# Optimization experiments

Hardware: AMD Instinct MI355X
Metric: run time of the kernel (lower is better)

## Reference

```python
import math
import jax, jax.numpy as jnp
import numpy as np

C1, D, NUM_HEADS, K_CH = 150, 32, 4, 10
GLOBAL_TOPK_RATIO = 0.08


def _pos2d(h, w, dim):
    d2 = dim // 2
    div = jnp.exp(jnp.arange(0, d2, 2, dtype=jnp.float32) * (-(math.log(10000.0) / d2)))
    def axis_pe(n):
        ang = jnp.arange(n, dtype=jnp.float32)[:, None] * div[None, :]
        pe = jnp.zeros((n, d2), dtype=jnp.float32)
        pe = pe.at[:, 0::2].set(jnp.sin(ang))
        pe = pe.at[:, 1::2].set(jnp.cos(ang))
        return pe
    pe_y = axis_pe(h)  # [h, d2]
    pe_x = axis_pe(w)  # [w, d2]
    return jnp.concatenate([
        jnp.broadcast_to(pe_y[:, None, :], (h, w, d2)),
        jnp.broadcast_to(pe_x[None, :, :], (h, w, d2)),
    ], axis=-1)  # [h, w, dim]


def setup_inputs() -> dict:
    key = jax.random.key(0)
    ks = jax.random.split(key, 7)
    B = 1024
    return {
        "x": jax.random.uniform(ks[0], (B, 1, 28, 28), dtype=jnp.float32),
        "conv1_w": jax.random.normal(ks[1], (C1, 1, 9, 9), dtype=jnp.float32) * 0.05,
        "channel_embed": jax.random.normal(ks[2], (C1, D), dtype=jnp.float32) * 0.02,
        "in_proj_w": jax.random.normal(ks[3], (3 * D, D), dtype=jnp.float32) * (1.0 / math.sqrt(D)),
        "in_proj_b": jnp.zeros((3 * D,), dtype=jnp.float32),
        "out_proj_w": jax.random.normal(ks[4], (D, D), dtype=jnp.float32) * (1.0 / math.sqrt(D)),
        "out_proj_b": jnp.zeros((D,), dtype=jnp.float32),
    }


def reference(x, conv1_w, channel_embed, in_proj_w, in_proj_b, out_proj_w, out_proj_b):
    # conv1 + relu: [B,1,28,28] -> [B,150,14,14]
    A = jax.nn.relu(jax.lax.conv_general_dilated(
        x, conv1_w, window_strides=(2, 2), padding=((4, 4), (4, 4)),
        dimension_numbers=("NCHW", "OIHW", "NCHW")))
    B, C, H, W = A.shape
    total = C * H * W
    k_global = max(1, int(math.ceil(GLOBAL_TOPK_RATIO * total)))
    A_flat = A.reshape(B, -1)
    # global kthvalue threshold: k_global-th largest per sample
    thresh = jax.lax.top_k(A_flat, k_global)[0][:, -1:]
    A_global = (A_flat * (A_flat >= thresh)).reshape(B, C, H, W)
    # per-location channel top-k + scatter
    v = jnp.transpose(A_global, (0, 2, 3, 1))  # [B,H,W,C]
    topv, topi = jax.lax.top_k(v, K_CH)        # [B,H,W,k]
    N = B * H * W
    logits = jnp.zeros((N, C), v.dtype).at[
        jnp.arange(N)[:, None], topi.reshape(N, K_CH)
    ].set(topv.reshape(N, K_CH)).reshape(v.shape)
    # normalize by per-sample global max (guard zero)
    flat_logits = logits.reshape(B, -1)
    gmax = jnp.max(flat_logits, axis=1, keepdims=True)
    normed = jnp.where(gmax == 0, 0.0, flat_logits / jnp.where(gmax == 0, 1.0, gmax))
    sparse_weights = normed.reshape(logits.shape)  # [B,H,W,C]
    # channel embedding + 2D sinusoidal PE
    loc_emb = jnp.einsum("bhwc,cd->bhwd", sparse_weights, channel_embed)
    loc_emb = loc_emb + _pos2d(H, W, D)[None]
    seq = loc_emb.reshape(B, H * W, D)
    # 1-layer MHA (self-attention, batch_first)
    qkv = seq @ in_proj_w.T + in_proj_b  # [B,S,3D]
    q, k, vv = jnp.split(qkv, 3, axis=-1)
    hd = D // NUM_HEADS
    def heads(t):
        return jnp.transpose(t.reshape(B, H * W, NUM_HEADS, hd), (0, 2, 1, 3))
    q, k, vv = heads(q), heads(k), heads(vv)
    attn = jax.nn.softmax(jnp.einsum("bnsd,bntd->bnst", q, k) / math.sqrt(hd), axis=-1)
    ctx = jnp.einsum("bnst,bntd->bnsd", attn, vv)
    ctx = jnp.transpose(ctx, (0, 2, 1, 3)).reshape(B, H * W, D)
    attn_out = ctx @ out_proj_w.T + out_proj_b  # [B, 196, 32]
    return attn_out
```

## Files before the change

### kernel.cpp

```cpp
#include <hip/hip_runtime.h>
#include <math.h>

#define NC1 150
#define HW 196
#define NB 1024
#define DD 32
#define NHD 4
#define HDIM 8
#define KG 2352
#define KCH 10
#define CAP 48
#define CVS 49
#define CES 36
#define KVS 20

#define UNI_F 17552
#define XT_OFF 0
#define WT_OFF 8232
#define CV_OFF 0
#define CC_OFF 9604
#define CNT_OFF 11956
#define CE_OFF 12152

__global__ void pos2d_kernel(float* __restrict__ pos) {
  int i = blockIdx.x * 256 + threadIdx.x;
  if (i >= HW * DD) return;
  int s = i >> 5, d = i & 31;
  int h = s / 14, w = s % 14;
  int p = (d < 16) ? h : w;
  int dd = (d < 16) ? d : d - 16;
  int j = dd >> 1;
  float dv = expf(-(logf(10000.0f) / 16.0f) * (float)(2 * j));
  float ang = (float)p * dv;
  pos[i] = (dd & 1) ? cosf(ang) : sinf(ang);
}

__global__ void prep_kernel(const float* __restrict__ cw, float* __restrict__ wtg) {
  int i = blockIdx.x * 256 + threadIdx.x;
  if (i >= 84 * 152) return;
  int k = i / 152, c = i - k * 152;
  wtg[i] = (k < 81 && c < NC1) ? cw[c * 81 + k] : 0.f;
}

__global__ __launch_bounds__(1024, 8) void fused_kernel(const float* __restrict__ x,
                                                        const float* __restrict__ wtg,
                                                        const float* __restrict__ CE,
                                                        const float* __restrict__ pos,
                                                        float* __restrict__ seqo) {
  __shared__ alignas(16) float uni[UNI_F];
  __shared__ alignas(16) float xs[784];
  __shared__ unsigned hist[2048];
  __shared__ unsigned wsum[4];
  __shared__ unsigned s_prefix, s_krem, s_max;

  int b = blockIdx.x, tid = threadIdx.x;
  int lane = tid & 63, wid = tid >> 6;

  if (tid < 196) ((float4*)xs)[tid] = ((const float4*)(x + (size_t)b * 784))[tid];
  if (tid == 0) { s_prefix = 0u; s_krem = KG; s_max = 0u; }
  __syncthreads();

  int cg = tid / 49;
  int g  = tid - cg * 49;
  bool act = (tid < 931);
  float acc[4][8];
#pragma unroll
  for (int i = 0; i < 4; ++i)
#pragma unroll
    for (int j = 0; j < 8; ++j) acc[i][j] = 0.f;

  float* XT = uni + XT_OFF;
  float* WT = uni + WT_OFF;

  for (int kb = 0; kb < 84; kb += 42) {
    for (int i = tid; i < 42 * 196; i += 1024) {
      int kk = i / 196, s = i - kk * 196;
      int k = kb + kk;
      float v = 0.f;
      if (k < 81) {
        int ki = k / 9, kj = k - ki * 9;
        int h = s / 14, w = s - h * 14;
        int r = 2 * h - 4 + ki, c = 2 * w - 4 + kj;
        if (r >= 0 && r < 28 && c >= 0 && c < 28) v = xs[r * 28 + c];
      }
      XT[i] = v;
    }
    for (int i = tid; i < (42 * 152) / 4; i += 1024)
      ((float4*)WT)[i] = ((const float4*)(wtg + kb * 152))[i];
    __syncthreads();
    if (act) {
      const float* xtp = XT + 4 * g;
      const float* wtp = WT + 8 * cg;
#pragma unroll 7
      for (int kk = 0; kk < 42; ++kk) {
        float4 xv = *(const float4*)(xtp + kk * 196);
        float4 w0 = *(const float4*)(wtp + kk * 152);
        float4 w1 = *(const float4*)(wtp + kk * 152 + 4);
        float xa[4] = {xv.x, xv.y, xv.z, xv.w};
        float wa[8] = {w0.x, w0.y, w0.z, w0.w, w1.x, w1.y, w1.z, w1.w};
#pragma unroll
        for (int i = 0; i < 4; ++i)
#pragma unroll
          for (int j = 0; j < 8; ++j) acc[i][j] += xa[i] * wa[j];
      }
    }
    __syncthreads();
  }

#pragma unroll
  for (int i = 0; i < 4; ++i)
#pragma unroll
    for (int j = 0; j < 8; ++j) acc[i][j] = fmaxf(acc[i][j], 0.f);

  for (int pass = 0; pass < 3; ++pass) {
    hist[tid] = 0u; hist[tid + 1024] = 0u;
    __syncthreads();
    int shift = (pass == 0) ? 21 : (pass == 1 ? 10 : 0);
    int bits = (pass == 2) ? 10 : 11;
    unsigned mask = (1u << bits) - 1u;
    unsigned pfx = s_prefix;
    unsigned krem = s_krem;
    int hishift = shift + bits;
    if (pass == 0) {
      unsigned mymax = 0u;
#pragma unroll
      for (int i = 0; i < 4; ++i)
#pragma unroll
        for (int j = 0; j < 8; ++j) {
          unsigned u = __float_as_uint(acc[i][j]);
          mymax = max(mymax, u);
          if (u) atomicAdd(&hist[u >> 21], 1u);
        }
#pragma unroll
      for (int st = 32; st >= 1; st >>= 1)
        mymax = max(mymax, (unsigned)__shfl_xor((int)mymax, st));
      if (lane == 0) atomicMax(&s_max, mymax);
    } else {
#pragma unroll
      for (int i = 0; i < 4; ++i)
#pragma unroll
        for (int j = 0; j < 8; ++j) {
          unsigned u = __float_as_uint(acc[i][j]);
          if (u && (u >> hishift) == pfx) atomicAdd(&hist[(u >> shift) & mask], 1u);
        }
    }
    __syncthreads();
    int segsz = (1 << bits) >> 8;
    unsigned segv = 0u, sufv = 0u;
    if (tid < 256) {
      for (int j = 0; j < segsz; ++j) segv += hist[tid * segsz + j];
      sufv = segv;
#pragma unroll
      for (int st = 1; st < 64; st <<= 1) {
        unsigned o = (unsigned)__shfl_down((int)sufv, st);
        if (lane + st < 64) sufv += o;
      }
      if (lane == 0) wsum[wid] = sufv;
    }
    __syncthreads();
    if (tid < 256) {
      unsigned tail = 0u;
      for (int ww = wid + 1; ww < 4; ++ww) tail += wsum[ww];
      sufv += tail;
      unsigned above = sufv - segv;
      if (above < krem && sufv >= krem) {
        unsigned cum = above;
        int dsel = tid * segsz;
        for (int d2 = segsz - 1; d2 >= 0; --d2) {
          int dd = tid * segsz + d2;
          if (cum + hist[dd] >= krem) { dsel = dd; break; }
          cum += hist[dd];
        }
        s_prefix = (pfx << bits) | (unsigned)dsel;
        s_krem = krem - cum;
      }
    }
    __syncthreads();
  }

  float* candV = uni + CV_OFF;
  unsigned char* candC = (unsigned char*)(uni + CC_OFF);
  unsigned* cnt = (unsigned*)(uni + CNT_OFF);
  if (tid < 196) cnt[tid] = 0u;
  __syncthreads();
  float T = __uint_as_float(s_prefix);
  if (act) {
#pragma unroll
    for (int i = 0; i < 4; ++i) {
      int loc = 4 * g + i;
#pragma unroll
      for (int j = 0; j < 8; ++j) {
        float v = acc[i][j];
        if (v >= T && v > 0.f) {
          unsigned slot = atomicAdd(&cnt[loc], 1u);
          if (slot < CAP) {
            candV[loc * CVS + slot] = v;
            candC[loc * CAP + slot] = (unsigned char)(8 * cg + j);
          }
        }
      }
    }
  }
  __syncthreads();

  float* CEs = uni + CE_OFF;
  if (tid >= 196) {
    for (int i = tid - 196; i < NC1 * 32; i += 1024 - 196) {
      int c = i >> 5, e = i & 31;
      CEs[c * CES + e] = CE[i];
    }
  }
  float tv[KCH]; int tc[KCH];
  if (tid < 196) {
    int loc = tid;
    unsigned n = cnt[loc]; if (n > CAP) n = CAP;
#pragma unroll
    for (int k = 0; k < KCH; ++k) { tv[k] = 0.f; tc[k] = 0; }
    for (unsigned jj = 0; jj < n; ++jj) {
      float v = candV[loc * CVS + jj];
      int c = candC[loc * CAP + jj];
      if (v > tv[KCH - 1] || (v == tv[KCH - 1] && c < tc[KCH - 1])) {
        float iv = v; int ic = c;
#pragma unroll
        for (int j = 0; j < KCH; ++j) {
          bool gt = (iv > tv[j]) || (iv == tv[j] && ic < tc[j]);
          float nv = gt ? iv : tv[j]; int nc = gt ? ic : tc[j];
          float ov = gt ? tv[j] : iv; int oc = gt ? tc[j] : ic;
          tv[j] = nv; tc[j] = nc; iv = ov; ic = oc;
        }
      }
    }
  }
  __syncthreads();

  if (tid < 196) {
    float gm = __uint_as_float(s_max);
    float gi = (gm == 0.0f) ? 0.0f : 1.0f / gm;
    float acc2[32];
#pragma unroll
    for (int e = 0; e < 32; ++e) acc2[e] = 0.f;
#pragma unroll
    for (int k = 0; k < KCH; ++k) {
      float v = tv[k];
      const float4* cr = (const float4*)(CEs + tc[k] * CES);
#pragma unroll
      for (int e4 = 0; e4 < 8; ++e4) {
        float4 cv = cr[e4];
        acc2[e4 * 4 + 0] += v * cv.x;
        acc2[e4 * 4 + 1] += v * cv.y;
        acc2[e4 * 4 + 2] += v * cv.z;
        acc2[e4 * 4 + 3] += v * cv.w;
      }
    }
    float* op = seqo + ((size_t)b * HW + tid) * DD;
    const float* pr = pos + tid * DD;
#pragma unroll
    for (int e4 = 0; e4 < 8; ++e4) {
      float4 pv = ((const float4*)pr)[e4];
      float4 o;
      o.x = acc2[e4 * 4 + 0] * gi + pv.x;
      o.y = acc2[e4 * 4 + 1] * gi + pv.y;
      o.z = acc2[e4 * 4 + 2] * gi + pv.z;
      o.w = acc2[e4 * 4 + 3] * gi + pv.w;
      ((float4*)op)[e4] = o;
    }
  }
}

__global__ __launch_bounds__(832, 3) void attn_kernel(const float* __restrict__ seq,
                                                      const float* __restrict__ Wqkv,
                                                      const float* __restrict__ bqkv,
                                                      float* __restrict__ ctxo) {
  __shared__ alignas(16) float kvs[NHD * HW * KVS];
  __shared__ alignas(16) float swq[96 * DD];
  __shared__ float sbq[96];
  __shared__ unsigned s_kk[NHD];

  int b = blockIdx.x, tid = threadIdx.x;
  int h = tid / HW;
  int s = tid - h * HW;
  bool act = (tid < NHD * HW);

  float xr[32];
  if (act) {
    const float* row = seq + ((size_t)b * HW + s) * DD;
#pragma unroll
    for (int e = 0; e < 8; ++e) {
      float4 f = ((const float4*)row)[e];
      xr[e * 4 + 0] = f.x; xr[e * 4 + 1] = f.y; xr[e * 4 + 2] = f.z; xr[e * 4 + 3] = f.w;
    }
  }
  for (int i = tid; i < (96 * DD) / 4; i += 832)
    ((float4*)swq)[i] = ((const float4*)Wqkv)[i];
  if (tid < 96) sbq[tid] = bqkv[tid];
  if (tid < NHD) s_kk[tid] = 0u;
  __syncthreads();

  float q[8]; float qq = 0.f;
  if (act) {
    float* kvrow = kvs + ((size_t)h * HW + s) * KVS;
    {
      float ka[8]; float kk = 0.f;
#pragma unroll
      for (int d = 0; d < 8; ++d) {
        const float* wr = swq + (32 + h * HDIM + d) * DD;
        float acc = sbq[32 + h * HDIM + d];
#pragma unroll
        for (int e = 0; e < DD; e += 4) {
          float4 wv = *(const float4*)(wr + e);
          acc += xr[e + 0] * wv.x + xr[e + 1] * wv.y + xr[e + 2] * wv.z + xr[e + 3] * wv.w;
        }
        ka[d] = acc; kk += acc * acc;
      }
      float4 k0 = {ka[0], ka[1], ka[2], ka[3]}, k1 = {ka[4], ka[5], ka[6], ka[7]};
      ((float4*)kvrow)[0] = k0; ((float4*)kvrow)[1] = k1;
      atomicMax(&s_kk[h], __float_as_uint(kk));
    }
    {
      float va[8];
#pragma unroll
      for (int d = 0; d < 8; ++d) {
        const float* wr = swq + (64 + h * HDIM + d) * DD;
        float acc = sbq[64 + h * HDIM + d];
#pragma unroll
        for (int e = 0; e < DD; e += 4) {
          float4 wv = *(const float4*)(wr + e);
          acc += xr[e + 0] * wv.x + xr[e + 1] * wv.y + xr[e + 2] * wv.z + xr[e + 3] * wv.w;
        }
        va[d] = acc;
      }
      float4 v0 = {va[0], va[1], va[2], va[3]}, v1 = {va[4], va[5], va[6], va[7]};
      ((float4*)kvrow)[2] = v0; ((float4*)kvrow)[3] = v1;
    }
#pragma unroll
    for (int d = 0; d < 8; ++d) {
      const float* wr = swq + (h * HDIM + d) * DD;
      float acc = sbq[h * HDIM + d];
#pragma unroll
      for (int e = 0; e < DD; e += 4) {
        float4 wv = *(const float4*)(wr + e);
        acc += xr[e + 0] * wv.x + xr[e + 1] * wv.y + xr[e + 2] * wv.z + xr[e + 3] * wv.w;
      }
      q[d] = acc; qq += acc * acc;
    }
  }
  __syncthreads();
  if (!act) return;

  const float scale = 0.3535533905932738f;
  float kkmax = __uint_as_float(s_kk[h]);
  float negM = -sqrtf(qq * kkmax) * scale;
  float l = 0.f;
  float c0 = 0.f, c1 = 0.f, c2 = 0.f, c3 = 0.f, c4 = 0.f, c5 = 0.f, c6 = 0.f, c7 = 0.f;
  const float4* kp = (const float4*)(kvs + (size_t)h * HW * KVS);
#pragma unroll 4
  for (int t = 0; t < HW; ++t) {
    float4 k0 = kp[0], k1 = kp[1], v0 = kp[2], v1 = kp[3];
    kp += 5;
    float sc = q[0] * k0.x;
    sc = fmaf(q[1], k0.y, sc); sc = fmaf(q[2], k0.z, sc); sc = fmaf(q[3], k0.w, sc);
    sc = fmaf(q[4], k1.x, sc); sc = fmaf(q[5], k1.y, sc); sc = fmaf(q[6], k1.z, sc);
    sc = fmaf(q[7], k1.w, sc);
    float p = __expf(fmaf(sc, scale, negM));
    l += p;
    c0 = fmaf(p, v0.x, c0); c1 = fmaf(p, v0.y, c1); c2 = fmaf(p, v0.z, c2);
    c3 = fmaf(p, v0.w, c3); c4 = fmaf(p, v1.x, c4); c5 = fmaf(p, v1.y, c5);
    c6 = fmaf(p, v1.z, c6); c7 = fmaf(p, v1.w, c7);
  }
  float inv = 1.0f / l;
  float* op = ctxo + ((size_t)b * HW + s) * DD + h * HDIM;
  float4 o0, o1;
  o0.x = c0 * inv; o0.y = c1 * inv; o0.z = c2 * inv; o0.w = c3 * inv;
  o1.x = c4 * inv; o1.y = c5 * inv; o1.z = c6 * inv; o1.w = c7 * inv;
  ((float4*)op)[0] = o0; ((float4*)op)[1] = o1;
}

__global__ __launch_bounds__(256) void outproj_kernel(const float* __restrict__ ctx,
                                                      const float* __restrict__ Wo,
                                                      const float* __restrict__ bo,
                                                      float* __restrict__ out) {
  __shared__ float sw[32 * 32];
  __shared__ float sb2[32];
  int tid = threadIdx.x;
  for (int i = tid; i < 1024; i += 256) sw[i] = Wo[i];
  if (tid < 32) sb2[tid] = bo[tid];
  __syncthreads();
  size_t row = (size_t)blockIdx.x * 256 + tid;
  const float* cr = ctx + row * 32;
  float xr[32];
#pragma unroll
  for (int e = 0; e < 8; ++e) {
    float4 f = ((const float4*)cr)[e];
    xr[e * 4 + 0] = f.x; xr[e * 4 + 1] = f.y; xr[e * 4 + 2] = f.z; xr[e * 4 + 3] = f.w;
  }
  float* op = out + row * 32;
#pragma unroll
  for (int d4 = 0; d4 < 8; ++d4) {
    float4 o;
    float* oo = (float*)&o;
#pragma unroll
    for (int q = 0; q < 4; ++q) {
      int d = d4 * 4 + q;
      float acc = sb2[d];
      const float* wr = sw + d * 32;
#pragma unroll
      for (int e = 0; e < 32; e += 4) {
        float4 wv = *(const float4*)(wr + e);
        acc += xr[e + 0] * wv.x + xr[e + 1] * wv.y + xr[e + 2] * wv.z + xr[e + 3] * wv.w;
      }
      oo[q] = acc;
    }
    ((float4*)op)[d4] = o;
  }
}

extern "C" void kernel_launch(void* const* d_in, const int* in_sizes, int n_in,
                              void* d_out, int out_size, void* d_ws, size_t ws_size,
                              hipStream_t stream) {
  const float* x  = (const float*)d_in[0];
  const float* cw = (const float*)d_in[1];
  const float* ce = (const float*)d_in[2];
  const float* wq = (const float*)d_in[3];
  const float* bq = (const float*)d_in[4];
  const float* wo = (const float*)d_in[5];
  const float* bo = (const float*)d_in[6];
  float* out = (float*)d_out;
  float* ws  = (float*)d_ws;

  float* ctx = ws;
  float* pos = ws + (size_t)NB * HW * DD;
  float* wtg = pos + HW * DD;

  prep_kernel<<<(84 * 152 + 255) / 256, 256, 0, stream>>>(cw, wtg);
  pos2d_kernel<<<(HW * DD + 255) / 256, 256, 0, stream>>>(pos);
  fused_kernel<<<NB, 1024, 0, stream>>>(x, wtg, ce, pos, out);
  attn_kernel<<<NB, 832, 0, stream>>>(out, wq, bq, ctx);
  outproj_kernel<<<(NB * HW * DD) / (256 * 32), 256, 0, stream>>>(ctx, wo, bo, out);
}
```

Baseline: 394.9 us.

## Merge prep kernels, prefetch K/V in attention loop, use exp2 and packed FMA

After: 401.2 us. No clear change (+1.6%).

```diff
diff --git a/kernel.cpp b/kernel.cpp
--- a/kernel.cpp
+++ b/kernel.cpp
@@ -14,6 +14,24 @@
 #define CES 36
 #define KVS 20
 
+typedef float v2f __attribute__((ext_vector_type(2)));
+
+__device__ __forceinline__ float dot32v(const v2f* __restrict__ xr2,
+                                        const float* __restrict__ wr, float bias) {
+  const float4* w4 = (const float4*)wr;
+  v2f s0 = {bias, 0.f};
+  v2f s1 = {0.f, 0.f};
+#pragma unroll
+  for (int e = 0; e < 8; ++e) {
+    float4 w = w4[e];
+    v2f wlo = {w.x, w.y}, whi = {w.z, w.w};
+    s0 = __builtin_elementwise_fma(xr2[2 * e], wlo, s0);
+    s1 = __builtin_elementwise_fma(xr2[2 * e + 1], whi, s1);
+  }
+  v2f s = s0 + s1;
+  return s.x + s.y;
+}
+
 #define UNI_F 17552
 #define XT_OFF 0
 #define WT_OFF 8232
@@ -22,24 +40,25 @@
 #define CNT_OFF 11956
 #define CE_OFF 12152
 
-__global__ void pos2d_kernel(float* __restrict__ pos) {
+__global__ void prep2_kernel(const float* __restrict__ cw, float* __restrict__ wtg,
+                             float* __restrict__ pos) {
   int i = blockIdx.x * 256 + threadIdx.x;
-  if (i >= HW * DD) return;
-  int s = i >> 5, d = i & 31;
-  int h = s / 14, w = s % 14;
-  int p = (d < 16) ? h : w;
-  int dd = (d < 16) ? d : d - 16;
-  int j = dd >> 1;
-  float dv = expf(-(logf(10000.0f) / 16.0f) * (float)(2 * j));
-  float ang = (float)p * dv;
-  pos[i] = (dd & 1) ? cosf(ang) : sinf(ang);
-}
-
-__global__ void prep_kernel(const float* __restrict__ cw, float* __restrict__ wtg) {
-  int i = blockIdx.x * 256 + threadIdx.x;
-  if (i >= 84 * 152) return;
-  int k = i / 152, c = i - k * 152;
-  wtg[i] = (k < 81 && c < NC1) ? cw[c * 81 + k] : 0.f;
+  if (i < HW * DD) {
+    int s = i >> 5, d = i & 31;
+    int h = s / 14, w = s % 14;
+    int p = (d < 16) ? h : w;
+    int dd = (d < 16) ? d : d - 16;
+    int j = dd >> 1;
+    float dv = expf(-(logf(10000.0f) / 16.0f) * (float)(2 * j));
+    float ang = (float)p * dv;
+    pos[i] = (dd & 1) ? cosf(ang) : sinf(ang);
+    return;
+  }
+  int j = i - HW * DD;
+  if (j < 84 * 152) {
+    int k = j / 152, c = j - k * 152;
+    wtg[j] = (k < 81 && c < NC1) ? cw[c * 81 + k] : 0.f;
+  }
 }
 
 __global__ __launch_bounds__(1024, 8) void fused_kernel(const float* __restrict__ x,
@@ -298,7 +317,7 @@
 
   float q[8]; float qq = 0.f;
   if (act) {
-    float* kvrow = kvs + ((size_t)h * HW + s) * KVS;
+    float* kvrow = kvs + (h * HW + s) * KVS;
     {
       float ka[8]; float kk = 0.f;
 #pragma unroll
@@ -347,21 +366,35 @@
   __syncthreads();
   if (!act) return;
 
-  const float scale = 0.3535533905932738f;
+  const float scaleL = 0.3535533905932738f * 1.4426950408889634f;
   float kkmax = __uint_as_float(s_kk[h]);
-  float negM = -sqrtf(qq * kkmax) * scale;
+  float negML = -sqrtf(qq * kkmax) * scaleL;
   float l = 0.f;
   float c0 = 0.f, c1 = 0.f, c2 = 0.f, c3 = 0.f, c4 = 0.f, c5 = 0.f, c6 = 0.f, c7 = 0.f;
-  const float4* kp = (const float4*)(kvs + (size_t)h * HW * KVS);
-#pragma unroll 4
-  for (int t = 0; t < HW; ++t) {
-    float4 k0 = kp[0], k1 = kp[1], v0 = kp[2], v1 = kp[3];
-    kp += 5;
+  const float4* kp = (const float4*)(kvs + (h * HW) * KVS);
+  float4 k0 = kp[0], k1 = kp[1], v0 = kp[2], v1 = kp[3];
+#pragma unroll 2
+  for (int t = 0; t < HW - 1; ++t) {
+    const float4* np = kp + 5;
+    float4 nk0 = np[0], nk1 = np[1], nv0 = np[2], nv1 = np[3];
     float sc = q[0] * k0.x;
     sc = fmaf(q[1], k0.y, sc); sc = fmaf(q[2], k0.z, sc); sc = fmaf(q[3], k0.w, sc);
     sc = fmaf(q[4], k1.x, sc); sc = fmaf(q[5], k1.y, sc); sc = fmaf(q[6], k1.z, sc);
     sc = fmaf(q[7], k1.w, sc);
-    float p = __expf(fmaf(sc, scale, negM));
+    float p = exp2f(fmaf(sc, scaleL, negML));
+    l += p;
+    c0 = fmaf(p, v0.x, c0); c1 = fmaf(p, v0.y, c1); c2 = fmaf(p, v0.z, c2);
+    c3 = fmaf(p, v0.w, c3); c4 = fmaf(p, v1.x, c4); c5 = fmaf(p, v1.y, c5);
+    c6 = fmaf(p, v1.z, c6); c7 = fmaf(p, v1.w, c7);
+    k0 = nk0; k1 = nk1; v0 = nv0; v1 = nv1;
+    kp = np;
+  }
+  {
+    float sc = q[0] * k0.x;
+    sc = fmaf(q[1], k0.y, sc); sc = fmaf(q[2], k0.z, sc); sc = fmaf(q[3], k0.w, sc);
+    sc = fmaf(q[4], k1.x, sc); sc = fmaf(q[5], k1.y, sc); sc = fmaf(q[6], k1.z, sc);
+    sc = fmaf(q[7], k1.w, sc);
+    float p = exp2f(fmaf(sc, scaleL, negML));
     l += p;
     c0 = fmaf(p, v0.x, c0); c1 = fmaf(p, v0.y, c1); c2 = fmaf(p, v0.z, c2);
     c3 = fmaf(p, v0.w, c3); c4 = fmaf(p, v1.x, c4); c5 = fmaf(p, v1.y, c5);
@@ -387,11 +420,12 @@
   __syncthreads();
   size_t row = (size_t)blockIdx.x * 256 + tid;
   const float* cr = ctx + row * 32;
-  float xr[32];
+  v2f xr2[16];
 #pragma unroll
   for (int e = 0; e < 8; ++e) {
     float4 f = ((const float4*)cr)[e];
-    xr[e * 4 + 0] = f.x; xr[e * 4 + 1] = f.y; xr[e * 4 + 2] = f.z; xr[e * 4 + 3] = f.w;
+    v2f lo = {f.x, f.y}, hi = {f.z, f.w};
+    xr2[2 * e] = lo; xr2[2 * e + 1] = hi;
   }
   float* op = out + row * 32;
 #pragma unroll
@@ -401,14 +435,7 @@
 #pragma unroll
     for (int q = 0; q < 4; ++q) {
       int d = d4 * 4 + q;
-      float acc = sb2[d];
-      const float* wr = sw + d * 32;
-#pragma unroll
-      for (int e = 0; e < 32; e += 4) {
-        float4 wv = *(const float4*)(wr + e);
-        acc += xr[e + 0] * wv.x + xr[e + 1] * wv.y + xr[e + 2] * wv.z + xr[e + 3] * wv.w;
-      }
-      oo[q] = acc;
+      oo[q] = dot32v(xr2, sw + d * 32, sb2[d]);
     }
     ((float4*)op)[d4] = o;
   }
@@ -431,8 +458,7 @@
   float* pos = ws + (size_t)NB * HW * DD;
   float* wtg = pos + HW * DD;
 
-  prep_kernel<<<(84 * 152 + 255) / 256, 256, 0, stream>>>(cw, wtg);
-  pos2d_kernel<<<(HW * DD + 255) / 256, 256, 0, stream>>>(pos);
+  prep2_kernel<<<(HW * DD + 84 * 152 + 255) / 256, 256, 0, stream>>>(cw, wtg, pos);
   fused_kernel<<<NB, 1024, 0, stream>>>(x, wtg, ce, pos, out);
   attn_kernel<<<NB, 832, 0, stream>>>(out, wq, bq, ctx);
   outproj_kernel<<<(NB * HW * DD) / (256 * 32), 256, 0, stream>>>(ctx, wo, bo, out);
```
